# Kernel optimization log

Hardware: AMD Instinct MI355X
Metric: run time of the kernel (lower is better)

The kernel has to match this reference:

```python
import jax, jax.numpy as jnp
import numpy as np

B = 1; H = 256; W = 256; C = 192; HEADS = 6; WS = 16; SHIFT = 8
N = WS * WS; HD = C // HEADS; HID = 4 * C


def setup_inputs() -> dict:
    key = jax.random.key(0)
    ks = jax.random.split(key, 8)
    # relative position index (standard Swin construction)
    coords = np.stack(np.meshgrid(np.arange(WS), np.arange(WS), indexing='ij'))  # 2,ws,ws
    cf = coords.reshape(2, -1)
    rel = (cf[:, :, None] - cf[:, None, :]).transpose(1, 2, 0)  # n,n,2
    rel[..., 0] += WS - 1
    rel[..., 1] += WS - 1
    rel[..., 0] *= 2 * WS - 1
    rpi = rel.sum(-1).astype(np.int32)  # [N,N], values in [0, (2*WS-1)^2)
    # shifted-window attention mask (standard Swin construction)
    img = np.zeros((1, H, W, 1), np.float32)
    cnt = 0
    sl = (slice(0, -WS), slice(-WS, -SHIFT), slice(-SHIFT, None))
    for hs in sl:
        for ws_ in sl:
            img[:, hs, ws_, :] = cnt
            cnt += 1
    mw = img.reshape(1, H // WS, WS, W // WS, WS, 1).transpose(0, 1, 3, 2, 4, 5).reshape(-1, N)
    diff = mw[:, None, :] - mw[:, :, None]  # [nw, N, N]
    attn_mask = np.where(diff != 0, np.float32(-100.0), np.float32(0.0))
    std = 0.02
    p = lambda k, shp: jax.random.normal(k, shp, jnp.float32) * std
    return {
        'x': jax.random.normal(ks[0], (B, H * W, C), jnp.float32),
        'rpi_sa': jnp.asarray(rpi),
        'attn_mask': jnp.asarray(attn_mask),
        'norm1_g': jnp.ones((C,), jnp.float32), 'norm1_b': jnp.zeros((C,), jnp.float32),
        'qkv_w': p(ks[1], (C, 3 * C)), 'qkv_b': jnp.zeros((3 * C,), jnp.float32),
        'rpb_table': p(ks[2], ((2 * WS - 1) * (2 * WS - 1), HEADS)),
        'proj_w': p(ks[3], (C, C)), 'proj_b': jnp.zeros((C,), jnp.float32),
        'norm2_g': jnp.ones((C,), jnp.float32), 'norm2_b': jnp.zeros((C,), jnp.float32),
        'fc1_w': p(ks[4], (C, HID)), 'fc1_b': jnp.zeros((HID,), jnp.float32),
        'fc2_w': p(ks[5], (HID, C)), 'fc2_b': jnp.zeros((C,), jnp.float32),
    }


def _ln(x, g, b):
    m = x.mean(-1, keepdims=True)
    v = ((x - m) ** 2).mean(-1, keepdims=True)
    return (x - m) * jax.lax.rsqrt(v + 1e-5) * g + b


def reference(x, rpi_sa, attn_mask, norm1_g, norm1_b, qkv_w, qkv_b, rpb_table,
              proj_w, proj_b, norm2_g, norm2_b, fc1_w, fc1_b, fc2_w, fc2_b):
    b = x.shape[0]
    shortcut = x
    h = _ln(x, norm1_g, norm1_b).reshape(b, H, W, C)
    h = jnp.roll(h, (-SHIFT, -SHIFT), axis=(1, 2))
    # window partition -> (b*nw, N, C)
    xw = h.reshape(b, H // WS, WS, W // WS, WS, C).transpose(0, 1, 3, 2, 4, 5).reshape(-1, N, C)
    qkv = (xw @ qkv_w + qkv_b).reshape(-1, N, 3, HEADS, HD).transpose(2, 0, 3, 1, 4)
    q, k, v = qkv[0] * (HD ** -0.5), qkv[1], qkv[2]  # [b_, H, N, HD]
    attn = jnp.einsum('bhnd,bhmd->bhnm', q, k)  # [b_, H, N, N]
    bias = rpb_table[rpi_sa.reshape(-1)].reshape(N, N, HEADS).transpose(2, 0, 1)
    attn = attn + bias[None]
    nw = attn_mask.shape[0]
    attn = attn.reshape(-1, nw, HEADS, N, N) + attn_mask[None, :, None]
    attn = jax.nn.softmax(attn.reshape(-1, HEADS, N, N), axis=-1)
    out = jnp.einsum('bhnm,bhmd->bnhd', attn, v).reshape(-1, N, C)
    out = out @ proj_w + proj_b
    # window reverse + unshift
    out = out.reshape(b, H // WS, W // WS, WS, WS, C).transpose(0, 1, 3, 2, 4, 5).reshape(b, H, W, C)
    out = jnp.roll(out, (SHIFT, SHIFT), axis=(1, 2)).reshape(b, H * W, C)
    xr = shortcut + out  # drop_path = identity (eval / drop_prob=0)
    y = _ln(xr, norm2_g, norm2_b)
    y = jax.nn.gelu(y @ fc1_w + fc1_b, approximate=False) @ fc2_w + fc2_b
    return xr + y
```

## Files before the change

### kernel.cpp

```cpp
#include <hip/hip_runtime.h>
#include <math.h>

#define NHEADS 6
#define CC 192
#define HDIM 32
#define NTOK 256
#define SHIFTV 8

typedef __attribute__((ext_vector_type(8))) short short8;
typedef __attribute__((ext_vector_type(4))) short short4v;
typedef __attribute__((ext_vector_type(4))) float floatx4;

__device__ inline short f2bf(float f) {
    union { float f; unsigned u; } v; v.f = f;
    unsigned r = (v.u + 0x7FFFu + ((v.u >> 16) & 1u)) >> 16;
    return (short)r;
}

__global__ __launch_bounds__(256) void bias_kernel(const int* __restrict__ rpi,
                                                   const float* __restrict__ rpb,
                                                   float* __restrict__ biasB) {
    int idx = blockIdx.x * 256 + threadIdx.x;
    int m = idx & 255;
    int n = (idx >> 8) & 255;
    int h = idx >> 16;
    biasB[idx] = rpb[rpi[n * 256 + m] * NHEADS + h];
}

__global__ __launch_bounds__(256) void cvt_kernel(const float* __restrict__ qkvw,
                                                  const float* __restrict__ pw,
                                                  const float* __restrict__ f1w,
                                                  const float* __restrict__ f2w,
                                                  short* __restrict__ wqt,
                                                  short* __restrict__ pwt,
                                                  short* __restrict__ w1t,
                                                  short* __restrict__ w2t) {
    int idx = blockIdx.x * 256 + threadIdx.x;
    int n = idx / 192, k = idx - n * 192;
    w1t[idx] = f2bf(f1w[k * 768 + n]);
    int c = idx / 768, h = idx - c * 768;
    w2t[idx] = f2bf(f2w[h * 192 + c]);
    if (idx < 576 * 192) wqt[idx] = f2bf(qkvw[k * 576 + n]);
    if (idx < 192 * 192) pwt[idx] = f2bf(pw[k * 192 + n]);
}

__global__ __launch_bounds__(256) void qkv_kernel(const float* __restrict__ x,
        const float* __restrict__ g1, const float* __restrict__ b1,
        const short* __restrict__ wqt, const float* __restrict__ qkvb,
        ushort* __restrict__ Qb, ushort* __restrict__ Kb, ushort* __restrict__ VTb) {
    __shared__ __align__(16) short xln[64 * 200];
    __shared__ float red[64][4][2];
    const int t = threadIdx.x;
    const int g0 = blockIdx.x * 64;
    const int w = g0 >> 8;
    {
        int row = t >> 2, part = t & 3;
        int n = (g0 + row) & 255;
        int sy = (((w >> 4) << 4) + (n >> 4) + SHIFTV) & 255;
        int sx = (((w & 15) << 4) + (n & 15) + SHIFTV) & 255;
        const float* xr = x + (sy * 256 + sx) * CC + part * 48;
        float vals[48];
        float s = 0.f, ss = 0.f;
        #pragma unroll
        for (int i = 0; i < 48; ++i) { float v = xr[i]; vals[i] = v; s += v; ss += v * v; }
        red[row][part][0] = s; red[row][part][1] = ss;
        __syncthreads();
        float sum = red[row][0][0] + red[row][1][0] + red[row][2][0] + red[row][3][0];
        float sq  = red[row][0][1] + red[row][1][1] + red[row][2][1] + red[row][3][1];
        float mean = sum * (1.f / 192.f);
        float var = sq * (1.f / 192.f) - mean * mean;
        float inv = rsqrtf(var + 1e-5f);
        #pragma unroll
        for (int i = 0; i < 48; ++i) {
            int c = part * 48 + i;
            xln[row * 200 + c] = f2bf((vals[i] - mean) * inv * g1[c] + b1[c]);
        }
    }
    __syncthreads();
    const int wv = t >> 6, lane = t & 63;
    const int lr = lane & 15;
    const int lk = (lane >> 4) * 8;
    const int q4 = (lane >> 4) * 4;
    #pragma unroll
    for (int jc = 0; jc < 3; ++jc) {
        floatx4 acc[4][3];
        #pragma unroll
        for (int mt = 0; mt < 4; ++mt)
            #pragma unroll
            for (int nt = 0; nt < 3; ++nt) acc[mt][nt] = floatx4{0.f,0.f,0.f,0.f};
        for (int ks = 0; ks < 6; ++ks) {
            int k0 = ks * 32 + lk;
            short8 a[4];
            #pragma unroll
            for (int mt = 0; mt < 4; ++mt)
                a[mt] = *(const short8*)&xln[(mt * 16 + lr) * 200 + k0];
            #pragma unroll
            for (int nt = 0; nt < 3; ++nt) {
                int nglob = jc * 192 + wv * 48 + nt * 16 + lr;
                short8 b = *(const short8*)&wqt[nglob * 192 + k0];
                #pragma unroll
                for (int mt = 0; mt < 4; ++mt)
                    acc[mt][nt] = __builtin_amdgcn_mfma_f32_16x16x32_bf16(a[mt], b, acc[mt][nt], 0, 0, 0);
            }
        }
        #pragma unroll
        for (int nt = 0; nt < 3; ++nt) {
            int jj = wv * 48 + nt * 16 + lr;
            float bias = qkvb[jc * 192 + jj];
            int head = jj >> 5, hd = jj & 31;
            int wh = w * NHEADS + head;
            #pragma unroll
            for (int mt = 0; mt < 4; ++mt) {
                int nr0 = (g0 + mt * 16 + q4) & 255;
                if (jc == 0) {
                    #pragma unroll
                    for (int reg = 0; reg < 4; ++reg)
                        Qb[((size_t)wh * NTOK + nr0 + reg) * HDIM + hd] =
                            (ushort)f2bf((acc[mt][nt][reg] + bias) * 0.17677669529663687f);
                } else if (jc == 1) {
                    #pragma unroll
                    for (int reg = 0; reg < 4; ++reg)
                        Kb[((size_t)wh * NTOK + nr0 + reg) * HDIM + hd] =
                            (ushort)f2bf(acc[mt][nt][reg] + bias);
                } else {
                    short4v pk;
                    #pragma unroll
                    for (int reg = 0; reg < 4; ++reg)
                        pk[reg] = f2bf(acc[mt][nt][reg] + bias);
                    *(short4v*)&VTb[((size_t)wh * HDIM + hd) * NTOK + nr0] = pk;
                }
            }
        }
    }
}

__global__ __launch_bounds__(256) void attn_kernel(const ushort* __restrict__ Q,
        const ushort* __restrict__ K, const ushort* __restrict__ VT,
        const float* __restrict__ biasB, const float* __restrict__ mask,
        ushort* __restrict__ Ob) {
    __shared__ __align__(16) ushort Ks[256 * 40];
    __shared__ __align__(16) ushort Vs[32 * 264];
    __shared__ __align__(16) ushort Ps[4][64 * 40];
    const int t = threadIdx.x;
    const int wh = blockIdx.x;
    const int w = wh / 6, h = wh - w * 6;
    {
        const ushort* kg = K + (size_t)wh * (NTOK * HDIM);
        const ushort* vg = VT + (size_t)wh * (NTOK * HDIM);
        for (int i = t * 8; i < NTOK * HDIM; i += 2048) {
            short8 kv = *(const short8*)(kg + i);
            *(short8*)&Ks[(i >> 5) * 40 + (i & 31)] = kv;
            short8 vv = *(const short8*)(vg + i);
            *(short8*)&Vs[(i >> 8) * 264 + (i & 255)] = vv;
        }
    }
    const int wv = t >> 6, lane = t & 63;
    const int lc = lane & 15;
    const int q4 = (lane >> 4) * 4;
    const int lk8 = (lane >> 4) * 8;
    const int qb = wv * 64;
    short8 qf[4];
    {
        const ushort* qg = Q + (size_t)wh * (NTOK * HDIM);
        #pragma unroll
        for (int qt = 0; qt < 4; ++qt)
            qf[qt] = *(const short8*)(qg + (qb + qt * 16 + lc) * HDIM + lk8);
    }
    __syncthreads();
    float M[4], Ssum[4];
    floatx4 o[2][4];
    #pragma unroll
    for (int qt = 0; qt < 4; ++qt) {
        M[qt] = -1e30f; Ssum[qt] = 0.f;
        o[0][qt] = floatx4{0.f,0.f,0.f,0.f};
        o[1][qt] = floatx4{0.f,0.f,0.f,0.f};
    }
    ushort* Pw = &Ps[wv][0];
    const float* bp = biasB + h * 65536;
    const float* mp = mask + (size_t)w * 65536;
    for (int kc = 0; kc < 8; ++kc) {
        const int k0 = kc * 32;
        short8 ka[2];
        ka[0] = *(const short8*)&Ks[(k0 + lc) * 40 + lk8];
        ka[1] = *(const short8*)&Ks[(k0 + 16 + lc) * 40 + lk8];
        floatx4 sf[2][4];
        #pragma unroll
        for (int kt = 0; kt < 2; ++kt)
            #pragma unroll
            for (int qt = 0; qt < 4; ++qt)
                sf[kt][qt] = __builtin_amdgcn_mfma_f32_16x16x32_bf16(ka[kt], qf[qt],
                                floatx4{0.f,0.f,0.f,0.f}, 0, 0, 0);
        #pragma unroll
        for (int kt = 0; kt < 2; ++kt)
            #pragma unroll
            for (int qt = 0; qt < 4; ++qt) {
                int q = qb + qt * 16 + lc;
                int kbase = k0 + kt * 16 + q4;
                float4 bb = *(const float4*)(bp + q * 256 + kbase);
                float4 mm = *(const float4*)(mp + q * 256 + kbase);
                sf[kt][qt][0] += bb.x + mm.x;
                sf[kt][qt][1] += bb.y + mm.y;
                sf[kt][qt][2] += bb.z + mm.z;
                sf[kt][qt][3] += bb.w + mm.w;
            }
        #pragma unroll
        for (int qt = 0; qt < 4; ++qt) {
            float mloc = sf[0][qt][0];
            #pragma unroll
            for (int r = 1; r < 4; ++r) mloc = fmaxf(mloc, sf[0][qt][r]);
            #pragma unroll
            for (int r = 0; r < 4; ++r) mloc = fmaxf(mloc, sf[1][qt][r]);
            mloc = fmaxf(mloc, __shfl_xor(mloc, 16));
            mloc = fmaxf(mloc, __shfl_xor(mloc, 32));
            float Mn = fmaxf(M[qt], mloc);
            float alpha = __expf(M[qt] - Mn);
            M[qt] = Mn;
            float rs = 0.f;
            #pragma unroll
            for (int kt = 0; kt < 2; ++kt) {
                #pragma unroll
                for (int r = 0; r < 4; ++r) {
                    float p = __expf(sf[kt][qt][r] - Mn);
                    sf[kt][qt][r] = p;
                    rs += p;
                }
            }
            rs += __shfl_xor(rs, 16);
            rs += __shfl_xor(rs, 32);
            Ssum[qt] = Ssum[qt] * alpha + rs;
            o[0][qt] *= alpha;
            o[1][qt] *= alpha;
            #pragma unroll
            for (int kt = 0; kt < 2; ++kt) {
                short4v pk;
                pk.x = f2bf(sf[kt][qt][0]);
                pk.y = f2bf(sf[kt][qt][1]);
                pk.z = f2bf(sf[kt][qt][2]);
                pk.w = f2bf(sf[kt][qt][3]);
                *(short4v*)&Pw[(qt * 16 + lc) * 40 + kt * 16 + q4] = pk;
            }
        }
        short8 va[2], pf[4];
        va[0] = *(const short8*)&Vs[lc * 264 + k0 + lk8];
        va[1] = *(const short8*)&Vs[(16 + lc) * 264 + k0 + lk8];
        #pragma unroll
        for (int qt = 0; qt < 4; ++qt)
            pf[qt] = *(const short8*)&Pw[(qt * 16 + lc) * 40 + lk8];
        #pragma unroll
        for (int ht = 0; ht < 2; ++ht)
            #pragma unroll
            for (int qt = 0; qt < 4; ++qt)
                o[ht][qt] = __builtin_amdgcn_mfma_f32_16x16x32_bf16(va[ht], pf[qt], o[ht][qt], 0, 0, 0);
    }
    #pragma unroll
    for (int qt = 0; qt < 4; ++qt) {
        float inv = 1.f / Ssum[qt];
        size_t rowbase = ((size_t)(w * NTOK + qb + qt * 16 + lc)) * CC + h * HDIM;
        #pragma unroll
        for (int ht = 0; ht < 2; ++ht)
            #pragma unroll
            for (int r = 0; r < 4; ++r)
                Ob[rowbase + ht * 16 + q4 + r] = (ushort)f2bf(o[ht][qt][r] * inv);
    }
}

__global__ __launch_bounds__(256) void proj_kernel(const ushort* __restrict__ Ob,
        const short* __restrict__ pwt, const float* __restrict__ pb,
        const float* __restrict__ x, float* __restrict__ out) {
    __shared__ __align__(16) short oln[64 * 200];
    const int t = threadIdx.x;
    const int g0 = blockIdx.x * 64;
    const int w = g0 >> 8;
    {
        int row = t >> 2, part = t & 3;
        const ushort* orow = Ob + (size_t)(g0 + row) * CC + part * 48;
        #pragma unroll
        for (int i = 0; i < 6; ++i)
            *(short8*)&oln[row * 200 + part * 48 + i * 8] = *(const short8*)(orow + i * 8);
    }
    __syncthreads();
    const int wv = t >> 6, lane = t & 63;
    const int lr = lane & 15;
    const int lk = (lane >> 4) * 8;
    const int q4 = (lane >> 4) * 4;
    floatx4 acc[4][3];
    #pragma unroll
    for (int mt = 0; mt < 4; ++mt)
        #pragma unroll
        for (int nt = 0; nt < 3; ++nt) acc[mt][nt] = floatx4{0.f,0.f,0.f,0.f};
    for (int ks = 0; ks < 6; ++ks) {
        int k0 = ks * 32 + lk;
        short8 a[4];
        #pragma unroll
        for (int mt = 0; mt < 4; ++mt)
            a[mt] = *(const short8*)&oln[(mt * 16 + lr) * 200 + k0];
        #pragma unroll
        for (int nt = 0; nt < 3; ++nt) {
            int c = wv * 48 + nt * 16 + lr;
            short8 b = *(const short8*)&pwt[c * 192 + k0];
            #pragma unroll
            for (int mt = 0; mt < 4; ++mt)
                acc[mt][nt] = __builtin_amdgcn_mfma_f32_16x16x32_bf16(a[mt], b, acc[mt][nt], 0, 0, 0);
        }
    }
    #pragma unroll
    for (int nt = 0; nt < 3; ++nt) {
        int c = wv * 48 + nt * 16 + lr;
        float bias = pb[c];
        #pragma unroll
        for (int mt = 0; mt < 4; ++mt) {
            #pragma unroll
            for (int reg = 0; reg < 4; ++reg) {
                int nn = (g0 + mt * 16 + q4 + reg) & 255;
                int sy = (((w >> 4) << 4) + (nn >> 4) + SHIFTV) & 255;
                int sx = (((w & 15) << 4) + (nn & 15) + SHIFTV) & 255;
                size_t base = (size_t)(sy * 256 + sx) * CC;
                out[base + c] = x[base + c] + acc[mt][nt][reg] + bias;
            }
        }
    }
}

__global__ __launch_bounds__(256) void mlp_kernel(const float* __restrict__ g2,
        const float* __restrict__ b2, const short* __restrict__ w1t,
        const float* __restrict__ f1b, const short* __restrict__ w2t,
        const float* __restrict__ f2b, float* __restrict__ out) {
    __shared__ __align__(16) short xln[64 * 200];
    __shared__ __align__(16) short Hs[64 * 136];
    __shared__ float red[64][4][2];
    const int t = threadIdx.x;
    const int m0 = blockIdx.x * 64;
    {
        int row = t >> 2, part = t & 3;
        const float* xr = out + (size_t)(m0 + row) * CC + part * 48;
        float vals[48];
        float s = 0.f, ss = 0.f;
        #pragma unroll
        for (int i = 0; i < 48; ++i) { float v = xr[i]; vals[i] = v; s += v; ss += v * v; }
        red[row][part][0] = s; red[row][part][1] = ss;
        __syncthreads();
        float sum = red[row][0][0] + red[row][1][0] + red[row][2][0] + red[row][3][0];
        float sq  = red[row][0][1] + red[row][1][1] + red[row][2][1] + red[row][3][1];
        float mean = sum * (1.f / 192.f);
        float var = sq * (1.f / 192.f) - mean * mean;
        float inv = rsqrtf(var + 1e-5f);
        #pragma unroll
        for (int i = 0; i < 48; ++i) {
            int c = part * 48 + i;
            xln[row * 200 + c] = f2bf((vals[i] - mean) * inv * g2[c] + b2[c]);
        }
    }
    __syncthreads();
    const int wv = t >> 6;
    const int lane = t & 63;
    const int lr = lane & 15;
    const int lk = (lane >> 4) * 8;
    const int q4 = (lane >> 4) * 4;
    floatx4 acc2[4][3];
    #pragma unroll
    for (int mt = 0; mt < 4; ++mt)
        #pragma unroll
        for (int nt = 0; nt < 3; ++nt) acc2[mt][nt] = floatx4{0.f, 0.f, 0.f, 0.f};

    for (int hc = 0; hc < 6; ++hc) {
        floatx4 acc1[4][2];
        #pragma unroll
        for (int mt = 0; mt < 4; ++mt)
            #pragma unroll
            for (int nt = 0; nt < 2; ++nt) acc1[mt][nt] = floatx4{0.f, 0.f, 0.f, 0.f};
        for (int ks = 0; ks < 6; ++ks) {
            int k0 = ks * 32 + lk;
            short8 a[4];
            #pragma unroll
            for (int mt = 0; mt < 4; ++mt)
                a[mt] = *(const short8*)&xln[(mt * 16 + lr) * 200 + k0];
            #pragma unroll
            for (int nt = 0; nt < 2; ++nt) {
                int n = hc * 128 + (wv * 2 + nt) * 16 + lr;
                short8 b = *(const short8*)&w1t[n * 192 + k0];
                #pragma unroll
                for (int mt = 0; mt < 4; ++mt)
                    acc1[mt][nt] = __builtin_amdgcn_mfma_f32_16x16x32_bf16(a[mt], b, acc1[mt][nt], 0, 0, 0);
            }
        }
        __syncthreads();
        #pragma unroll
        for (int nt = 0; nt < 2; ++nt) {
            int colb = (wv * 2 + nt) * 16 + lr;
            float bias = f1b[hc * 128 + colb];
            #pragma unroll
            for (int mt = 0; mt < 4; ++mt) {
                #pragma unroll
                for (int reg = 0; reg < 4; ++reg) {
                    float v = acc1[mt][nt][reg] + bias;
                    float gl = 0.5f * v * (1.f + erff(v * 0.70710678118654752f));
                    Hs[(mt * 16 + q4 + reg) * 136 + colb] = f2bf(gl);
                }
            }
        }
        __syncthreads();
        for (int ks = 0; ks < 4; ++ks) {
            int k0 = ks * 32 + lk;
            short8 a[4];
            #pragma unroll
            for (int mt = 0; mt < 4; ++mt)
                a[mt] = *(const short8*)&Hs[(mt * 16 + lr) * 136 + k0];
            #pragma unroll
            for (int nt = 0; nt < 3; ++nt) {
                int c = wv * 48 + nt * 16 + lr;
                short8 b = *(const short8*)&w2t[c * 768 + hc * 128 + k0];
                #pragma unroll
                for (int mt = 0; mt < 4; ++mt)
                    acc2[mt][nt] = __builtin_amdgcn_mfma_f32_16x16x32_bf16(a[mt], b, acc2[mt][nt], 0, 0, 0);
            }
        }
    }
    #pragma unroll
    for (int nt = 0; nt < 3; ++nt) {
        int c = wv * 48 + nt * 16 + lr;
        float bias = f2b[c];
        #pragma unroll
        for (int mt = 0; mt < 4; ++mt) {
            #pragma unroll
            for (int reg = 0; reg < 4; ++reg) {
                size_t off = (size_t)(m0 + mt * 16 + q4 + reg) * CC + c;
                out[off] = out[off] + acc2[mt][nt][reg] + bias;
            }
        }
    }
}

extern "C" void kernel_launch(void* const* d_in, const int* in_sizes, int n_in,
                              void* d_out, int out_size, void* d_ws, size_t ws_size,
                              hipStream_t stream) {
    (void)in_sizes; (void)n_in; (void)out_size; (void)ws_size;
    const float* x    = (const float*)d_in[0];
    const int*   rpi  = (const int*)d_in[1];
    const float* mask = (const float*)d_in[2];
    const float* n1g  = (const float*)d_in[3];
    const float* n1b  = (const float*)d_in[4];
    const float* qkvw = (const float*)d_in[5];
    const float* qkvb = (const float*)d_in[6];
    const float* rpb  = (const float*)d_in[7];
    const float* pw   = (const float*)d_in[8];
    const float* pb   = (const float*)d_in[9];
    const float* n2g  = (const float*)d_in[10];
    const float* n2b  = (const float*)d_in[11];
    const float* f1w  = (const float*)d_in[12];
    const float* f1b  = (const float*)d_in[13];
    const float* f2w  = (const float*)d_in[14];
    const float* f2b  = (const float*)d_in[15];
    float* out = (float*)d_out;

    ushort* Qb  = (ushort*)d_ws;
    ushort* Kb  = Qb + 12582912;
    ushort* VTb = Kb + 12582912;
    ushort* Ob  = VTb + 12582912;
    float* BIAS = (float*)(Ob + 12582912);
    short* WQT  = (short*)(BIAS + 393216);
    short* PWT  = WQT + 110592;
    short* W1T  = PWT + 36864;
    short* W2T  = W1T + 147456;

    bias_kernel<<<1536, 256, 0, stream>>>(rpi, rpb, BIAS);
    cvt_kernel<<<576, 256, 0, stream>>>(qkvw, pw, f1w, f2w, WQT, PWT, W1T, W2T);
    qkv_kernel<<<1024, 256, 0, stream>>>(x, n1g, n1b, WQT, qkvb, Qb, Kb, VTb);
    attn_kernel<<<1536, 256, 0, stream>>>(Qb, Kb, VTb, BIAS, mask, Ob);
    proj_kernel<<<1024, 256, 0, stream>>>(Ob, PWT, pb, x, out);
    mlp_kernel<<<1024, 256, 0, stream>>>(n2g, n2b, W1T, f1b, W2T, f2b, out);
}
```

Baseline: 495.2 us.

## Drop online softmax max tracking, approximate GELU, widen MLP hidden chunk

Attention now exponentiates biased logits directly without running-max tracking or rescaling, and reduces row sums across lanes only once at the end. MLP GELU switches from erf to a tanh-style sigmoid approximation using exp and a fast reciprocal. The MLP hidden dimension is processed in 4 chunks of 192 instead of 6 of 128, with a larger shared buffer. Risks are overflow if logits are large and a small GELU accuracy change.

```diff
diff --git a/kernel.cpp b/kernel.cpp
--- a/kernel.cpp
+++ b/kernel.cpp
@@ -15,6 +15,13 @@
     union { float f; unsigned u; } v; v.f = f;
     unsigned r = (v.u + 0x7FFFu + ((v.u >> 16) & 1u)) >> 16;
     return (short)r;
+}
+
+__device__ inline float gelu_f(float x) {
+    float x2 = x * x;
+    float p = x * (-1.5957691216f - 0.07135481627f * x2);
+    float e = __expf(p);
+    return x * __builtin_amdgcn_rcpf(1.f + e);
 }
 
 __global__ __launch_bounds__(256) void bias_kernel(const int* __restrict__ rpi,
@@ -167,11 +174,11 @@
             qf[qt] = *(const short8*)(qg + (qb + qt * 16 + lc) * HDIM + lk8);
     }
     __syncthreads();
-    float M[4], Ssum[4];
+    float Ssum[4];
     floatx4 o[2][4];
     #pragma unroll
     for (int qt = 0; qt < 4; ++qt) {
-        M[qt] = -1e30f; Ssum[qt] = 0.f;
+        Ssum[qt] = 0.f;
         o[0][qt] = floatx4{0.f,0.f,0.f,0.f};
         o[1][qt] = floatx4{0.f,0.f,0.f,0.f};
     }
@@ -198,48 +205,15 @@
                 int kbase = k0 + kt * 16 + q4;
                 float4 bb = *(const float4*)(bp + q * 256 + kbase);
                 float4 mm = *(const float4*)(mp + q * 256 + kbase);
-                sf[kt][qt][0] += bb.x + mm.x;
-                sf[kt][qt][1] += bb.y + mm.y;
-                sf[kt][qt][2] += bb.z + mm.z;
-                sf[kt][qt][3] += bb.w + mm.w;
-            }
-        #pragma unroll
-        for (int qt = 0; qt < 4; ++qt) {
-            float mloc = sf[0][qt][0];
-            #pragma unroll
-            for (int r = 1; r < 4; ++r) mloc = fmaxf(mloc, sf[0][qt][r]);
-            #pragma unroll
-            for (int r = 0; r < 4; ++r) mloc = fmaxf(mloc, sf[1][qt][r]);
-            mloc = fmaxf(mloc, __shfl_xor(mloc, 16));
-            mloc = fmaxf(mloc, __shfl_xor(mloc, 32));
-            float Mn = fmaxf(M[qt], mloc);
-            float alpha = __expf(M[qt] - Mn);
-            M[qt] = Mn;
-            float rs = 0.f;
-            #pragma unroll
-            for (int kt = 0; kt < 2; ++kt) {
-                #pragma unroll
-                for (int r = 0; r < 4; ++r) {
-                    float p = __expf(sf[kt][qt][r] - Mn);
-                    sf[kt][qt][r] = p;
-                    rs += p;
-                }
-            }
-            rs += __shfl_xor(rs, 16);
-            rs += __shfl_xor(rs, 32);
-            Ssum[qt] = Ssum[qt] * alpha + rs;
-            o[0][qt] *= alpha;
-            o[1][qt] *= alpha;
-            #pragma unroll
-            for (int kt = 0; kt < 2; ++kt) {
+                float p0 = __expf(sf[kt][qt][0] + bb.x + mm.x);
+                float p1 = __expf(sf[kt][qt][1] + bb.y + mm.y);
+                float p2 = __expf(sf[kt][qt][2] + bb.z + mm.z);
+                float p3 = __expf(sf[kt][qt][3] + bb.w + mm.w);
+                Ssum[qt] += (p0 + p1) + (p2 + p3);
                 short4v pk;
-                pk.x = f2bf(sf[kt][qt][0]);
-                pk.y = f2bf(sf[kt][qt][1]);
-                pk.z = f2bf(sf[kt][qt][2]);
-                pk.w = f2bf(sf[kt][qt][3]);
+                pk.x = f2bf(p0); pk.y = f2bf(p1); pk.z = f2bf(p2); pk.w = f2bf(p3);
                 *(short4v*)&Pw[(qt * 16 + lc) * 40 + kt * 16 + q4] = pk;
             }
-        }
         short8 va[2], pf[4];
         va[0] = *(const short8*)&Vs[lc * 264 + k0 + lk8];
         va[1] = *(const short8*)&Vs[(16 + lc) * 264 + k0 + lk8];
@@ -254,7 +228,10 @@
     }
     #pragma unroll
     for (int qt = 0; qt < 4; ++qt) {
-        float inv = 1.f / Ssum[qt];
+        float rs = Ssum[qt];
+        rs += __shfl_xor(rs, 16);
+        rs += __shfl_xor(rs, 32);
+        float inv = 1.f / rs;
         size_t rowbase = ((size_t)(w * NTOK + qb + qt * 16 + lc)) * CC + h * HDIM;
         #pragma unroll
         for (int ht = 0; ht < 2; ++ht)
@@ -326,7 +303,7 @@
         const float* __restrict__ f1b, const short* __restrict__ w2t,
         const float* __restrict__ f2b, float* __restrict__ out) {
     __shared__ __align__(16) short xln[64 * 200];
-    __shared__ __align__(16) short Hs[64 * 136];
+    __shared__ __align__(16) short Hs[64 * 200];
     __shared__ float red[64][4][2];
     const int t = threadIdx.x;
     const int m0 = blockIdx.x * 64;
@@ -362,12 +339,12 @@
         #pragma unroll
         for (int nt = 0; nt < 3; ++nt) acc2[mt][nt] = floatx4{0.f, 0.f, 0.f, 0.f};
 
-    for (int hc = 0; hc < 6; ++hc) {
-        floatx4 acc1[4][2];
+    for (int hc = 0; hc < 4; ++hc) {
+        floatx4 acc1[4][3];
         #pragma unroll
         for (int mt = 0; mt < 4; ++mt)
             #pragma unroll
-            for (int nt = 0; nt < 2; ++nt) acc1[mt][nt] = floatx4{0.f, 0.f, 0.f, 0.f};
+            for (int nt = 0; nt < 3; ++nt) acc1[mt][nt] = floatx4{0.f, 0.f, 0.f, 0.f};
         for (int ks = 0; ks < 6; ++ks) {
             int k0 = ks * 32 + lk;
             short8 a[4];
@@ -375,8 +352,8 @@
             for (int mt = 0; mt < 4; ++mt)
                 a[mt] = *(const short8*)&xln[(mt * 16 + lr) * 200 + k0];
             #pragma unroll
-            for (int nt = 0; nt < 2; ++nt) {
-                int n = hc * 128 + (wv * 2 + nt) * 16 + lr;
+            for (int nt = 0; nt < 3; ++nt) {
+                int n = hc * 192 + wv * 48 + nt * 16 + lr;
                 short8 b = *(const short8*)&w1t[n * 192 + k0];
                 #pragma unroll
                 for (int mt = 0; mt < 4; ++mt)
@@ -385,30 +362,29 @@
         }
         __syncthreads();
         #pragma unroll
-        for (int nt = 0; nt < 2; ++nt) {
-            int colb = (wv * 2 + nt) * 16 + lr;
-            float bias = f1b[hc * 128 + colb];
+        for (int nt = 0; nt < 3; ++nt) {
+            int colb = wv * 48 + nt * 16 + lr;
+            float bias = f1b[hc * 192 + colb];
             #pragma unroll
             for (int mt = 0; mt < 4; ++mt) {
                 #pragma unroll
                 for (int reg = 0; reg < 4; ++reg) {
                     float v = acc1[mt][nt][reg] + bias;
-                    float gl = 0.5f * v * (1.f + erff(v * 0.70710678118654752f));
-                    Hs[(mt * 16 + q4 + reg) * 136 + colb] = f2bf(gl);
+                    Hs[(mt * 16 + q4 + reg) * 200 + colb] = f2bf(gelu_f(v));
                 }
             }
         }
         __syncthreads();
-        for (int ks = 0; ks < 4; ++ks) {
+        for (int ks = 0; ks < 6; ++ks) {
             int k0 = ks * 32 + lk;
             short8 a[4];
             #pragma unroll
             for (int mt = 0; mt < 4; ++mt)
-                a[mt] = *(const short8*)&Hs[(mt * 16 + lr) * 136 + k0];
+                a[mt] = *(const short8*)&Hs[(mt * 16 + lr) * 200 + k0];
             #pragma unroll
             for (int nt = 0; nt < 3; ++nt) {
                 int c = wv * 48 + nt * 16 + lr;
-                short8 b = *(const short8*)&w2t[c * 768 + hc * 128 + k0];
+                short8 b = *(const short8*)&w2t[c * 768 + hc * 192 + k0];
                 #pragma unroll
                 for (int mt = 0; mt < 4; ++mt)
                     acc2[mt][nt] = __builtin_amdgcn_mfma_f32_16x16x32_bf16(a[mt], b, acc2[mt][nt], 0, 0, 0);
```

Result: faster. 484.3 us (-2.2%).
